# Performance work log

Measured on AMD Instinct MI355X. Metric: run time of the kernel, lower is better.

## Reference

```python
import jax, jax.numpy as jnp
import numpy as np

N, E, G = 10000, 160000, 64     # nodes, edges, graphs in batch
T, F_IN, F_OUT, L = 5, 75, 15, 4  # towers, per-tower in (divide_input=False), per-tower out, conv layers
AVG_DEG_LOG = float(np.log(17.0))  # stand-in for PyG histogram stat (source deg=zeros -> NaN)
BN_EPS = 1e-5
STD_EPS = 1e-5


def _u(key, shape):
    fi, fo = shape[-2], shape[-1]
    lim = float(np.sqrt(6.0 / (fi + fo)))
    return jax.random.uniform(key, shape, jnp.float32, -lim, lim)


def setup_inputs():
    key = jax.random.key(0)
    k = iter(jax.random.split(key, 24))
    inp = {}
    inp["x"] = jax.random.randint(next(k), (N, 2), 0, 21)
    inp["edge_index"] = jax.random.randint(next(k), (2, E), 0, N)
    inp["edge_attr"] = jax.random.randint(next(k), (E, 2), 0, 4)
    inp["batch"] = jnp.sort(jax.random.randint(next(k), (N,), 0, G))
    inp["node_emb"] = jax.random.normal(next(k), (21, 75), jnp.float32)
    inp["edge_emb"] = jax.random.normal(next(k), (4, 25), jnp.float32)
    inp["pre_lin_W"] = _u(next(k), (150, 75)); inp["pre_lin_b"] = jnp.zeros((75,), jnp.float32)
    inp["edge_enc_W"] = _u(next(k), (L, 50, F_IN)); inp["edge_enc_b"] = jnp.zeros((L, F_IN), jnp.float32)
    inp["pre_W"] = _u(next(k), (L, T, 3 * F_IN, F_IN)); inp["pre_b"] = jnp.zeros((L, T, F_IN), jnp.float32)
    inp["post_W"] = _u(next(k), (L, T, 13 * F_IN, F_OUT)); inp["post_b"] = jnp.zeros((L, T, F_OUT), jnp.float32)
    inp["lin_W"] = _u(next(k), (L, T * F_OUT, 75)); inp["lin_b"] = jnp.zeros((L, 75), jnp.float32)
    inp["bn_g"] = jnp.ones((L, 75), jnp.float32); inp["bn_b"] = jnp.zeros((L, 75), jnp.float32)
    inp["mlp_W1"] = _u(next(k), (75, 50)); inp["mlp_b1"] = jnp.zeros((50,), jnp.float32)
    inp["mlp_W2"] = _u(next(k), (50, 25)); inp["mlp_b2"] = jnp.zeros((25,), jnp.float32)
    inp["mlp_W3"] = _u(next(k), (25, 1)); inp["mlp_b3"] = jnp.zeros((1,), jnp.float32)
    return inp


def _forward(x, edge_index, edge_attr, batch, node_emb, edge_emb, pre_lin_W, pre_lin_b,
             edge_enc_W, edge_enc_b, pre_W, pre_b, post_W, post_b, lin_W, lin_b,
             bn_g, bn_b, mlp_W1, mlp_b1, mlp_W2, mlp_b2, mlp_W3, mlp_b3):
    # node / edge embeddings -> features
    h = node_emb[x].reshape(N, 150) @ pre_lin_W + pre_lin_b          # [N,75]
    ea = edge_emb[edge_attr].reshape(E, 50)                           # [E,50]
    src, dst = edge_index[0], edge_index[1]  # messages flow src -> dst (x_j=src, x_i=dst)

    cnt = jax.ops.segment_sum(jnp.ones((E,), jnp.float32), dst, num_segments=N)  # in-degree [N]
    deg = jnp.maximum(cnt, 1.0)[:, None, None]
    log_deg = jnp.log(jnp.maximum(cnt, 1.0) + 1.0)[:, None, None]
    amp = log_deg / AVG_DEG_LOG
    att = AVG_DEG_LOG / log_deg
    has = (cnt > 0)[:, None, None]

    for l in range(L):
        e = ea @ edge_enc_W[l] + edge_enc_b[l]                        # [E,75]
        m_in = jnp.concatenate([h[dst], h[src], e], axis=-1)          # [E,225]
        msgs = jnp.einsum('ec,tcf->etf', m_in, pre_W[l]) + pre_b[l]   # [E,T,75]
        s = jax.ops.segment_sum(msgs, dst, num_segments=N)
        mean = s / deg
        mean_sq = jax.ops.segment_sum(msgs * msgs, dst, num_segments=N) / deg
        std = jnp.sqrt(jax.nn.relu(mean_sq - mean * mean) + STD_EPS)
        mn = jnp.where(has, jax.ops.segment_min(msgs, dst, num_segments=N), 0.0)
        mx = jnp.where(has, jax.ops.segment_max(msgs, dst, num_segments=N), 0.0)
        agg = jnp.concatenate([mean, mn, mx, std], axis=-1)           # [N,T,300]
        scaled = jnp.concatenate([agg, agg * amp, agg * att], axis=-1)  # [N,T,900]
        out = jnp.concatenate([jnp.broadcast_to(h[:, None, :], (N, T, F_IN)), scaled], axis=-1)  # [N,T,975]
        post = jnp.einsum('ntc,tcf->ntf', out, post_W[l]) + post_b[l]  # [N,T,15]
        hc = post.reshape(N, T * F_OUT) @ lin_W[l] + lin_b[l]          # [N,75]
        mu = hc.mean(axis=0)
        var = hc.var(axis=0)  # biased, matches BatchNorm1d training mode
        h = jax.nn.relu((hc - mu) / jnp.sqrt(var + BN_EPS) * bn_g[l] + bn_b[l])

    g = jax.ops.segment_sum(h, batch, num_segments=G)                 # global_add_pool [G,75]
    g = jax.nn.relu(g @ mlp_W1 + mlp_b1)
    g = jax.nn.relu(g @ mlp_W2 + mlp_b2)
    return g @ mlp_W3 + mlp_b3                                        # [G,1]


def reference(x, edge_index, edge_attr, batch, node_emb, edge_emb, pre_lin_W, pre_lin_b,
              edge_enc_W, edge_enc_b, pre_W, pre_b, post_W, post_b, lin_W, lin_b,
              bn_g, bn_b, mlp_W1, mlp_b1, mlp_W2, mlp_b2, mlp_W3, mlp_b3):
    return _forward(x, edge_index, edge_attr, batch, node_emb, edge_emb, pre_lin_W, pre_lin_b,
                    edge_enc_W, edge_enc_b, pre_W, pre_b, post_W, post_b, lin_W, lin_b,
                    bn_g, bn_b, mlp_W1, mlp_b1, mlp_W2, mlp_b2, mlp_W3, mlp_b3)
```

## Files before the change

### kernel.cpp

```cpp
#include <hip/hip_runtime.h>
#include <hip/hip_bf16.h>
#include <math.h>

#define NN 10000
#define NE 160000
#define NG 64
#define NT 5
#define NL 4
#define ADL 2.833213344056216f

#define OFF_H      0
#define OFF_HC     750000
#define OFF_P      1500000
#define OFF_Q      5250000
#define OFF_AGG    9000000
#define OFF_RLUT   24000000
#define OFF_INVDEG 24006000
#define OFF_AMP    24016000
#define OFF_ATT    24026000
#define OFF_STATS  24036000
#define OFF_GPOOL  24036160
#define OFF_INT    24118960

__device__ __forceinline__ float bf2f(__hip_bfloat16 v){ return __bfloat162float(v); }

__global__ void k_zero_cnt(int* cnt){
    int i = blockIdx.x*256 + threadIdx.x;
    if (i < NN) cnt[i] = 0;
}

__global__ __launch_bounds__(256) void k_h0(const int* __restrict__ x,
        const float* __restrict__ node_emb, const float* __restrict__ plW,
        const float* __restrict__ plb, float* __restrict__ h){
    __shared__ float s_emb[21*75];
    __shared__ float s_W[150*75];
    __shared__ float s_b[75];
    int tid = threadIdx.x;
    for (int i = tid; i < 21*75; i += 256) s_emb[i] = node_emb[i];
    for (int i = tid; i < 150*75; i += 256) s_W[i] = plW[i];
    if (tid < 75) s_b[tid] = plb[tid];
    __syncthreads();
    for (int out = blockIdx.x*256 + tid; out < NN*75; out += gridDim.x*256){
        int n = out / 75, f = out - n*75;
        int x0 = x[2*n], x1 = x[2*n+1];
        float acc = s_b[f];
        const float* e0 = s_emb + x0*75;
        const float* e1 = s_emb + x1*75;
        #pragma unroll 5
        for (int k = 0; k < 75; k++)
            acc += e0[k]*s_W[k*75+f] + e1[k]*s_W[(75+k)*75+f];
        h[out] = acc;
    }
}

__global__ void k_hist(const int* __restrict__ ei, int* __restrict__ cnt){
    int e = blockIdx.x*256 + threadIdx.x;
    if (e < NE) atomicAdd(&cnt[ei[NE + e]], 1);
}

__global__ void k_scan(const int* __restrict__ cnt, int* __restrict__ eoff){
    __shared__ int buf[256];
    __shared__ int carry;
    int tid = threadIdx.x;
    if (tid == 0){ carry = 0; eoff[0] = 0; }
    __syncthreads();
    for (int base = 0; base < NN; base += 256){
        int v = (base + tid < NN) ? cnt[base + tid] : 0;
        buf[tid] = v; __syncthreads();
        for (int off = 1; off < 256; off <<= 1){
            int t2 = (tid >= off) ? buf[tid - off] : 0;
            __syncthreads();
            buf[tid] += t2;
            __syncthreads();
        }
        int inc = buf[tid] + carry;
        if (base + tid < NN) eoff[base + tid + 1] = inc;
        __syncthreads();
        if (tid == 255) carry = inc;
        __syncthreads();
    }
}

__global__ void k_nodestats(const int* __restrict__ cnt, const int* __restrict__ eoff,
        float* __restrict__ invdeg, float* __restrict__ amp, float* __restrict__ att,
        int* __restrict__ cursor){
    int n = blockIdx.x*256 + threadIdx.x;
    if (n >= NN) return;
    int c = cnt[n];
    cursor[n] = eoff[n];
    float cf = (float)c;
    float dg = cf < 1.f ? 1.f : cf;
    invdeg[n] = 1.f / dg;
    float ld = logf(dg + 1.f);
    amp[n] = ld / ADL;
    att[n] = ADL / ld;
}

__global__ void k_scatter(const int* __restrict__ ei, const int* __restrict__ ea,
        int* __restrict__ cursor, int* __restrict__ esrc, int* __restrict__ ecombo){
    int e = blockIdx.x*256 + threadIdx.x;
    if (e >= NE) return;
    int src = ei[e], dst = ei[NE + e];
    int pos = atomicAdd(&cursor[dst], 1);
    esrc[pos] = src;
    ecombo[pos] = ea[2*e]*4 + ea[2*e+1];
}

__global__ __launch_bounds__(384) void k_pq(const float* __restrict__ h,
        const float* __restrict__ preW, const float* __restrict__ preb,
        const float* __restrict__ edge_emb, const float* __restrict__ encW,
        const float* __restrict__ encb, int l,
        float* __restrict__ P, float* __restrict__ Q,
        float* __restrict__ Rlut, float* __restrict__ stats){
    __shared__ float smem[10675];
    int tid = threadIdx.x;
    int bx = blockIdx.x;

    if (bx == 318){
        for (int i = tid; i < 150; i += 384) stats[i] = 0.f;
        return;
    }
    if (bx >= 313){
        int t = bx - 313;
        float* s_encW = smem;
        float* s_ev   = smem + 3750;
        float* s_wc   = smem + 4950;
        float* s_ee   = smem + 10575;
        for (int i = tid; i < 3750; i += 384) s_encW[i] = encW[(size_t)l*3750 + i];
        for (int i = tid; i < 100; i += 384) s_ee[i] = edge_emb[i];
        const float* wcsrc = preW + (((size_t)(l*NT + t))*225 + 150)*75;
        for (int i = tid; i < 5625; i += 384) s_wc[i] = wcsrc[i];
        __syncthreads();
        for (int task = tid; task < 1200; task += 384){
            int b = task/75, m = task - 75*b;
            int a0 = b >> 2, a1 = b & 3;
            float s = encb[l*75 + m];
            for (int k = 0; k < 25; k++)
                s += s_ee[a0*25+k]*s_encW[k*75+m] + s_ee[a1*25+k]*s_encW[(25+k)*75+m];
            s_ev[task] = s;
        }
        __syncthreads();
        for (int task = tid; task < 1200; task += 384){
            int b = task/75, f = task - 75*b;
            float r = preb[((size_t)l*NT + t)*75 + f];
            const float* ev = s_ev + b*75;
            #pragma unroll 5
            for (int m = 0; m < 75; m++) r += ev[m]*s_wc[m*75 + f];
            Rlut[b*375 + t*75 + f] = r;
        }
        return;
    }

    float* h_t = smem;
    int base = bx*32;
    for (int idx = tid; idx < 32*75; idx += 384){
        int i = idx/75, m = idx - 75*i;
        int n = base + i;
        h_t[i*76 + m] = (n < NN) ? h[(size_t)n*75 + m] : 0.f;
    }
    __syncthreads();
    int j = tid;
    if (j >= 375) return;
    int t = j/75, f = j - 75*t;
    const float* wbase = preW + ((size_t)(l*NT + t))*225*75 + f;
    float accP[32], accQ[32];
    #pragma unroll
    for (int i = 0; i < 32; i++){ accP[i] = 0.f; accQ[i] = 0.f; }
    for (int m = 0; m < 72; m += 4){
        float wa0 = wbase[(m+0)*75], wa1 = wbase[(m+1)*75];
        float wa2 = wbase[(m+2)*75], wa3 = wbase[(m+3)*75];
        float wb0 = wbase[(75+m+0)*75], wb1 = wbase[(75+m+1)*75];
        float wb2 = wbase[(75+m+2)*75], wb3 = wbase[(75+m+3)*75];
        #pragma unroll
        for (int i = 0; i < 32; i++){
            const float4 hv = *(const float4*)&h_t[i*76 + m];
            accP[i] += hv.x*wa0 + hv.y*wa1 + hv.z*wa2 + hv.w*wa3;
            accQ[i] += hv.x*wb0 + hv.y*wb1 + hv.z*wb2 + hv.w*wb3;
        }
    }
    for (int m = 72; m < 75; m++){
        float wa = wbase[m*75], wb = wbase[(75+m)*75];
        #pragma unroll
        for (int i = 0; i < 32; i++){
            float v = h_t[i*76 + m];
            accP[i] += v*wa; accQ[i] += v*wb;
        }
    }
    for (int i = 0; i < 32; i++){
        int n = base + i;
        if (n < NN){ P[(size_t)n*375 + j] = accP[i]; Q[(size_t)n*375 + j] = accQ[i]; }
    }
}

#define JS 47
__global__ __launch_bounds__(64) void k_agg(const float* __restrict__ P,
        const float* __restrict__ Q, const float* __restrict__ Rlut,
        const int* __restrict__ eoff, const int* __restrict__ esrc,
        const int* __restrict__ ecombo, const float* __restrict__ invdeg,
        __hip_bfloat16* __restrict__ agg){
    int n = blockIdx.y;
    int j = blockIdx.x*JS + threadIdx.x;
    if (threadIdx.x >= JS || j >= 375) return;
    int lo = eoff[n], hi = eoff[n+1];
    float p = P[(size_t)n*375 + j];
    float sum = 0.f, sq = 0.f, mn = 3.4e38f, mx = -3.4e38f;
    int e = lo;
    for (; e + 4 <= hi; e += 4){
        int s0 = esrc[e],   s1 = esrc[e+1],   s2 = esrc[e+2],   s3 = esrc[e+3];
        int c0 = ecombo[e], c1 = ecombo[e+1], c2 = ecombo[e+2], c3 = ecombo[e+3];
        float q0 = Q[(size_t)s0*375 + j];
        float q1 = Q[(size_t)s1*375 + j];
        float q2 = Q[(size_t)s2*375 + j];
        float q3 = Q[(size_t)s3*375 + j];
        float r0 = Rlut[c0*375 + j];
        float r1 = Rlut[c1*375 + j];
        float r2 = Rlut[c2*375 + j];
        float r3 = Rlut[c3*375 + j];
        float m0 = p + q0 + r0, m1 = p + q1 + r1;
        float m2 = p + q2 + r2, m3 = p + q3 + r3;
        sum += m0 + m1 + m2 + m3;
        sq  += m0*m0 + m1*m1 + m2*m2 + m3*m3;
        mn = fminf(mn, fminf(fminf(m0, m1), fminf(m2, m3)));
        mx = fmaxf(mx, fmaxf(fmaxf(m0, m1), fmaxf(m2, m3)));
    }
    for (; e < hi; e++){
        int s = esrc[e], cm = ecombo[e];
        float m = p + Q[(size_t)s*375 + j] + Rlut[cm*375 + j];
        sum += m; sq += m*m;
        mn = fminf(mn, m); mx = fmaxf(mx, m);
    }
    float id = invdeg[n];
    bool has = hi > lo;
    float mean = sum*id;
    float msq  = sq*id;
    float var = msq - mean*mean; var = var > 0.f ? var : 0.f;
    float sd = sqrtf(var + 1e-5f);
    float mnv = has ? mn : 0.f;
    float mxv = has ? mx : 0.f;
    int t = j/75, f = j - 75*t;
    __hip_bfloat16* a = agg + ((size_t)n*NT + t)*300;
    a[f]      = __float2bfloat16(mean);
    a[75+f]   = __float2bfloat16(mnv);
    a[150+f]  = __float2bfloat16(mxv);
    a[225+f]  = __float2bfloat16(sd);
}

#define TK 25
#define PADA 27
__global__ __launch_bounds__(256, 4) void k_post(const float* __restrict__ h,
        const __hip_bfloat16* __restrict__ agg, const float* __restrict__ postW,
        const float* __restrict__ postb, const float* __restrict__ amp,
        const float* __restrict__ att, int l, float* __restrict__ postbase){
    __shared__ float s_a[256*PADA];
    __shared__ float s_w[3][TK*16];
    int t = blockIdx.y;
    int z = blockIdx.z;
    int nbase = blockIdx.x*256;
    int tid = threadIdx.x;
    int fg  = (tid & 3)*4;
    int sub = tid >> 2;
    const float* Wt = postW + ((size_t)(l*NT + t))*975*15;
    float a1[4][4], a2[4][4], a3[4][4];
    #pragma unroll
    for (int j = 0; j < 4; j++)
        #pragma unroll
        for (int f = 0; f < 4; f++){ a1[j][f]=0.f; a2[j][f]=0.f; a3[j][f]=0.f; }

    if (z == 0){
        for (int kt = 0; kt < 75; kt += TK){
            for (int idx = tid; idx < 256*TK; idx += 256){
                int row = idx / TK, c = idx - row*TK;
                int n = nbase + row;
                s_a[row*PADA + c] = (n < NN) ? h[(size_t)n*75 + kt + c] : 0.f;
            }
            for (int idx = tid; idx < TK*16; idx += 256){
                int c = idx >> 4, f = idx & 15;
                s_w[0][idx] = (f < 15) ? Wt[(kt + c)*15 + f] : 0.f;
            }
            __syncthreads();
            for (int k = 0; k < TK; k++){
                const float4 w1 = *(const float4*)&s_w[0][k*16 + fg];
                #pragma unroll
                for (int j = 0; j < 4; j++){
                    float v = s_a[(sub + 64*j)*PADA + k];
                    a1[j][0] += v*w1.x; a1[j][1] += v*w1.y;
                    a1[j][2] += v*w1.z; a1[j][3] += v*w1.w;
                }
            }
            __syncthreads();
        }
        const float* pb = postb + (l*NT + t)*15;
        #pragma unroll
        for (int j = 0; j < 4; j++){
            int n = nbase + sub + 64*j;
            if (n >= NN) continue;
            float* dst = postbase + (size_t)n*75 + t*15;
            #pragma unroll
            for (int f = 0; f < 4; f++)
                if (fg + f < 15) dst[fg + f] = a1[j][f] + pb[fg + f];
        }
        return;
    }

    int kbeg = (z-1)*50, kend = kbeg + 50;
    for (int kt = kbeg; kt < kend; kt += TK){
        for (int idx = tid; idx < 256*TK; idx += 256){
            int row = idx / TK, c = idx - row*TK;
            int n = nbase + row;
            s_a[row*PADA + c] = (n < NN) ?
                bf2f(agg[(size_t)n*1500 + t*300 + kt + c]) : 0.f;
        }
        for (int idx = tid; idx < TK*16; idx += 256){
            int c = idx >> 4, f = idx & 15;
            float v1 = 0.f, v2 = 0.f, v3 = 0.f;
            if (f < 15){
                v1 = Wt[( 75 + kt + c)*15 + f];
                v2 = Wt[(375 + kt + c)*15 + f];
                v3 = Wt[(675 + kt + c)*15 + f];
            }
            s_w[0][idx] = v1; s_w[1][idx] = v2; s_w[2][idx] = v3;
        }
        __syncthreads();
        for (int k = 0; k < TK; k++){
            const float4 w1 = *(const float4*)&s_w[0][k*16 + fg];
            const float4 w2 = *(const float4*)&s_w[1][k*16 + fg];
            const float4 w3 = *(const float4*)&s_w[2][k*16 + fg];
            #pragma unroll
            for (int j = 0; j < 4; j++){
                float v = s_a[(sub + 64*j)*PADA + k];
                a1[j][0] += v*w1.x; a1[j][1] += v*w1.y;
                a1[j][2] += v*w1.z; a1[j][3] += v*w1.w;
                a2[j][0] += v*w2.x; a2[j][1] += v*w2.y;
                a2[j][2] += v*w2.z; a2[j][3] += v*w2.w;
                a3[j][0] += v*w3.x; a3[j][1] += v*w3.y;
                a3[j][2] += v*w3.z; a3[j][3] += v*w3.w;
            }
        }
        __syncthreads();
    }

    float* postv = postbase + (size_t)z*750000;
    #pragma unroll
    for (int j = 0; j < 4; j++){
        int n = nbase + sub + 64*j;
        if (n >= NN) continue;
        float am = amp[n], at = att[n];
        float* dst = postv + (size_t)n*75 + t*15;
        #pragma unroll
        for (int f = 0; f < 4; f++)
            if (fg + f < 15)
                dst[fg + f] = a1[j][f] + am*a2[j][f] + at*a3[j][f];
    }
}

__global__ __launch_bounds__(256) void k_lin(const float* __restrict__ postbase,
        const float* __restrict__ linW, const float* __restrict__ linb,
        int l, float* __restrict__ hc, float* __restrict__ stats){
    __shared__ float p_l[32*75];
    __shared__ float w_l[75*75];
    __shared__ float hc_l[32*75];
    int tid = threadIdx.x;
    int base = blockIdx.x*32;
    for (int i = tid; i < 75*75; i += 256) w_l[i] = linW[(size_t)l*5625 + i];
    for (int i = tid; i < 32*75; i += 256){
        int n = base + i/75;
        size_t idx = (size_t)base*75 + i;
        float v = 0.f;
        if (n < NN){
            #pragma unroll
            for (int z = 0; z < 7; z++) v += postbase[idx + (size_t)z*750000];
        }
        p_l[i] = v;
    }
    __syncthreads();
    for (int task = tid; task < 2400; task += 256){
        int i = task/75, o = task - 75*i;
        float s = linb[l*75 + o];
        const float* pl = p_l + i*75;
        #pragma unroll 5
        for (int j = 0; j < 75; j++) s += pl[j]*w_l[j*75 + o];
        hc_l[task] = s;
        if (base + i < NN) hc[(size_t)(base+i)*75 + o] = s;
    }
    __syncthreads();
    if (tid < 75){
        int nv = NN - base; if (nv > 32) nv = 32;
        float s1 = 0.f, s2 = 0.f;
        for (int i = 0; i < nv; i++){
            float v = hc_l[i*75 + tid];
            s1 += v; s2 += v*v;
        }
        atomicAdd(&stats[tid], s1);
        atomicAdd(&stats[75+tid], s2);
    }
}

__global__ void k_bnapply(const float* __restrict__ hc, const float* __restrict__ stats,
        const float* __restrict__ bng, const float* __restrict__ bnb, int l,
        float* __restrict__ h){
    int idx = blockIdx.x*256 + threadIdx.x;
    if (idx >= NN*75) return;
    int col = idx % 75;
    float mu = stats[col]*(1.0f/NN);
    float var = stats[75+col]*(1.0f/NN) - mu*mu;
    float inv = rsqrtf(var + 1e-5f);
    float v = (hc[idx] - mu)*inv*bng[l*75+col] + bnb[l*75+col];
    h[idx] = v > 0.f ? v : 0.f;
}

__global__ __launch_bounds__(256) void k_pool(const float* __restrict__ h,
        const int* __restrict__ batch, float* __restrict__ gpool){
    int g = blockIdx.x, tid = threadIdx.x;
    int lo = 0, hi = NN;
    while (lo < hi){ int mid = (lo+hi)>>1; if (batch[mid] < g) lo = mid+1; else hi = mid; }
    int start = lo;
    lo = start; hi = NN;
    while (lo < hi){ int mid = (lo+hi)>>1; if (batch[mid] < g+1) lo = mid+1; else hi = mid; }
    int end = lo;
    __shared__ float red[225];
    if (tid < 225){
        int col = tid % 75, rep = tid / 75;
        float acc = 0.f;
        for (int i = start + rep; i < end; i += 3) acc += h[(size_t)i*75 + col];
        red[tid] = acc;
    }
    __syncthreads();
    if (tid < 75) gpool[g*75 + tid] = red[tid] + red[75+tid] + red[150+tid];
}

__global__ __launch_bounds__(256) void k_mlp(const float* __restrict__ gpool,
        const float* __restrict__ W1, const float* __restrict__ b1,
        const float* __restrict__ W2, const float* __restrict__ b2,
        const float* __restrict__ W3, const float* __restrict__ b3,
        float* __restrict__ out){
    __shared__ float w1[75*50];
    __shared__ float w2[50*25];
    __shared__ float gp[8*75];
    __shared__ float t1[8*50];
    __shared__ float t2[8*25];
    int tid = threadIdx.x;
    int gbase = blockIdx.x*8;
    for (int i = tid; i < 75*50; i += 256) w1[i] = W1[i];
    for (int i = tid; i < 50*25; i += 256) w2[i] = W2[i];
    for (int i = tid; i < 8*75; i += 256) gp[i] = gpool[gbase*75 + i];
    __syncthreads();
    for (int task = tid; task < 8*50; task += 256){
        int g = task/50, j = task - 50*g;
        float s = b1[j];
        const float* gv = gp + g*75;
        #pragma unroll 5
        for (int k = 0; k < 75; k++) s += gv[k]*w1[k*50+j];
        t1[task] = s > 0.f ? s : 0.f;
    }
    __syncthreads();
    for (int task = tid; task < 8*25; task += 256){
        int g = task/25, j = task - 25*g;
        float s = b2[j];
        const float* tv = t1 + g*50;
        #pragma unroll 5
        for (int k = 0; k < 50; k++) s += tv[k]*w2[k*25+j];
        t2[task] = s > 0.f ? s : 0.f;
    }
    __syncthreads();
    if (tid < 8){
        float s = b3[0];
        const float* tv = t2 + tid*25;
        #pragma unroll
        for (int k = 0; k < 25; k++) s += tv[k]*W3[k];
        out[gbase + tid] = s;
    }
}

extern "C" void kernel_launch(void* const* d_in, const int* in_sizes, int n_in,
                              void* d_out, int out_size, void* d_ws, size_t ws_size,
                              hipStream_t stream){
    const int* x          = (const int*)d_in[0];
    const int* edge_index = (const int*)d_in[1];
    const int* edge_attr  = (const int*)d_in[2];
    const int* batch      = (const int*)d_in[3];
    const float* node_emb = (const float*)d_in[4];
    const float* edge_emb = (const float*)d_in[5];
    const float* pre_lin_W= (const float*)d_in[6];
    const float* pre_lin_b= (const float*)d_in[7];
    const float* encW     = (const float*)d_in[8];
    const float* encb     = (const float*)d_in[9];
    const float* preW     = (const float*)d_in[10];
    const float* preb     = (const float*)d_in[11];
    const float* postW    = (const float*)d_in[12];
    const float* postb    = (const float*)d_in[13];
    const float* linW     = (const float*)d_in[14];
    const float* linb     = (const float*)d_in[15];
    const float* bng      = (const float*)d_in[16];
    const float* bnb      = (const float*)d_in[17];
    const float* mlpW1    = (const float*)d_in[18];
    const float* mlpb1    = (const float*)d_in[19];
    const float* mlpW2    = (const float*)d_in[20];
    const float* mlpb2    = (const float*)d_in[21];
    const float* mlpW3    = (const float*)d_in[22];
    const float* mlpb3    = (const float*)d_in[23];

    float* ws = (float*)d_ws;
    float* h      = ws + OFF_H;
    float* hc     = ws + OFF_HC;
    float* P      = ws + OFF_P;
    float* Q      = ws + OFF_Q;
    __hip_bfloat16* agg = (__hip_bfloat16*)(ws + OFF_AGG);
    float* Rlut   = ws + OFF_RLUT;
    float* invdeg = ws + OFF_INVDEG;
    float* amp    = ws + OFF_AMP;
    float* att    = ws + OFF_ATT;
    float* stats  = ws + OFF_STATS;
    float* gpool  = ws + OFF_GPOOL;
    float* postbase = ws + OFF_P;
    int* iw     = (int*)(ws + OFF_INT);
    int* cnt    = iw;
    int* eoff   = cnt + NN;
    int* cursor = eoff + NN + 2;
    int* esrc   = cursor + NN;
    int* ecombo = esrc + NE;

    k_zero_cnt<<<40, 256, 0, stream>>>(cnt);
    k_h0<<<640, 256, 0, stream>>>(x, node_emb, pre_lin_W, pre_lin_b, h);
    k_hist<<<625, 256, 0, stream>>>(edge_index, cnt);
    k_scan<<<1, 256, 0, stream>>>(cnt, eoff);
    k_nodestats<<<40, 256, 0, stream>>>(cnt, eoff, invdeg, amp, att, cursor);
    k_scatter<<<625, 256, 0, stream>>>(edge_index, edge_attr, cursor, esrc, ecombo);

    for (int l = 0; l < NL; l++){
        k_pq<<<319, 384, 0, stream>>>(h, preW, preb, edge_emb, encW, encb, l,
                                      P, Q, Rlut, stats);
        k_agg<<<dim3(8, NN), 64, 0, stream>>>(P, Q, Rlut, eoff, esrc, ecombo, invdeg, agg);
        k_post<<<dim3(40, 5, 7), 256, 0, stream>>>(h, agg, postW, postb, amp, att, l, postbase);
        k_lin<<<313, 256, 0, stream>>>(postbase, linW, linb, l, hc, stats);
        k_bnapply<<<2930, 256, 0, stream>>>(hc, stats, bng, bnb, l, h);
    }

    k_pool<<<NG, 256, 0, stream>>>(h, batch, gpool);
    k_mlp<<<8, 256, 0, stream>>>(gpool, mlpW1, mlpb1, mlpW2, mlpb2, mlpW3, mlpb3, (float*)d_out);
}
```

Baseline: 958.8 us.

## Store P/Q in bf16, widen agg unroll, drop LDS staging in post

The per-node pre-projections P and Q are now written and gathered as bf16 instead of fp32, halving the bytes moved by the gather-heavy aggregation kernel. The aggregation loop is unrolled to eight edges, and the grid uses full 64-thread blocks (6 per node) instead of 47 active lanes (8 per node). The post kernel stops staging activation tiles in shared memory and reads rows directly from global memory. Weights are loaded once into LDS and occupancy is raised to 6 blocks per CU. This trades extra rounding error in the messages, and uncoalesced per-thread row reads in the post kernel, for less memory traffic and fewer barriers.

```diff
diff --git a/kernel.cpp b/kernel.cpp
--- a/kernel.cpp
+++ b/kernel.cpp
@@ -110,7 +110,7 @@
         const float* __restrict__ preW, const float* __restrict__ preb,
         const float* __restrict__ edge_emb, const float* __restrict__ encW,
         const float* __restrict__ encb, int l,
-        float* __restrict__ P, float* __restrict__ Q,
+        __hip_bfloat16* __restrict__ P, __hip_bfloat16* __restrict__ Q,
         float* __restrict__ Rlut, float* __restrict__ stats){
     __shared__ float smem[10675];
     int tid = threadIdx.x;
@@ -188,44 +188,56 @@
     }
     for (int i = 0; i < 32; i++){
         int n = base + i;
-        if (n < NN){ P[(size_t)n*375 + j] = accP[i]; Q[(size_t)n*375 + j] = accQ[i]; }
-    }
-}
-
-#define JS 47
-__global__ __launch_bounds__(64) void k_agg(const float* __restrict__ P,
-        const float* __restrict__ Q, const float* __restrict__ Rlut,
+        if (n < NN){
+            P[(size_t)n*375 + j] = __float2bfloat16(accP[i]);
+            Q[(size_t)n*375 + j] = __float2bfloat16(accQ[i]);
+        }
+    }
+}
+
+__global__ __launch_bounds__(64) void k_agg(const __hip_bfloat16* __restrict__ P,
+        const __hip_bfloat16* __restrict__ Q, const float* __restrict__ Rlut,
         const int* __restrict__ eoff, const int* __restrict__ esrc,
         const int* __restrict__ ecombo, const float* __restrict__ invdeg,
         __hip_bfloat16* __restrict__ agg){
     int n = blockIdx.y;
-    int j = blockIdx.x*JS + threadIdx.x;
-    if (threadIdx.x >= JS || j >= 375) return;
+    int j = blockIdx.x*64 + threadIdx.x;
+    if (j >= 375) return;
     int lo = eoff[n], hi = eoff[n+1];
-    float p = P[(size_t)n*375 + j];
+    float p = bf2f(P[(size_t)n*375 + j]);
     float sum = 0.f, sq = 0.f, mn = 3.4e38f, mx = -3.4e38f;
     int e = lo;
-    for (; e + 4 <= hi; e += 4){
-        int s0 = esrc[e],   s1 = esrc[e+1],   s2 = esrc[e+2],   s3 = esrc[e+3];
-        int c0 = ecombo[e], c1 = ecombo[e+1], c2 = ecombo[e+2], c3 = ecombo[e+3];
-        float q0 = Q[(size_t)s0*375 + j];
-        float q1 = Q[(size_t)s1*375 + j];
-        float q2 = Q[(size_t)s2*375 + j];
-        float q3 = Q[(size_t)s3*375 + j];
-        float r0 = Rlut[c0*375 + j];
-        float r1 = Rlut[c1*375 + j];
-        float r2 = Rlut[c2*375 + j];
-        float r3 = Rlut[c3*375 + j];
+    for (; e + 8 <= hi; e += 8){
+        int s0 = esrc[e],   s1 = esrc[e+1], s2 = esrc[e+2], s3 = esrc[e+3];
+        int s4 = esrc[e+4], s5 = esrc[e+5], s6 = esrc[e+6], s7 = esrc[e+7];
+        int c0 = ecombo[e],   c1 = ecombo[e+1], c2 = ecombo[e+2], c3 = ecombo[e+3];
+        int c4 = ecombo[e+4], c5 = ecombo[e+5], c6 = ecombo[e+6], c7 = ecombo[e+7];
+        float q0 = bf2f(Q[(size_t)s0*375 + j]);
+        float q1 = bf2f(Q[(size_t)s1*375 + j]);
+        float q2 = bf2f(Q[(size_t)s2*375 + j]);
+        float q3 = bf2f(Q[(size_t)s3*375 + j]);
+        float q4 = bf2f(Q[(size_t)s4*375 + j]);
+        float q5 = bf2f(Q[(size_t)s5*375 + j]);
+        float q6 = bf2f(Q[(size_t)s6*375 + j]);
+        float q7 = bf2f(Q[(size_t)s7*375 + j]);
+        float r0 = Rlut[c0*375 + j], r1 = Rlut[c1*375 + j];
+        float r2 = Rlut[c2*375 + j], r3 = Rlut[c3*375 + j];
+        float r4 = Rlut[c4*375 + j], r5 = Rlut[c5*375 + j];
+        float r6 = Rlut[c6*375 + j], r7 = Rlut[c7*375 + j];
         float m0 = p + q0 + r0, m1 = p + q1 + r1;
         float m2 = p + q2 + r2, m3 = p + q3 + r3;
-        sum += m0 + m1 + m2 + m3;
-        sq  += m0*m0 + m1*m1 + m2*m2 + m3*m3;
-        mn = fminf(mn, fminf(fminf(m0, m1), fminf(m2, m3)));
-        mx = fmaxf(mx, fmaxf(fmaxf(m0, m1), fmaxf(m2, m3)));
+        float m4 = p + q4 + r4, m5 = p + q5 + r5;
+        float m6 = p + q6 + r6, m7 = p + q7 + r7;
+        sum += (m0 + m1 + m2 + m3) + (m4 + m5 + m6 + m7);
+        sq  += (m0*m0 + m1*m1 + m2*m2 + m3*m3) + (m4*m4 + m5*m5 + m6*m6 + m7*m7);
+        mn = fminf(mn, fminf(fminf(fminf(m0,m1), fminf(m2,m3)),
+                             fminf(fminf(m4,m5), fminf(m6,m7))));
+        mx = fmaxf(mx, fmaxf(fmaxf(fmaxf(m0,m1), fmaxf(m2,m3)),
+                             fmaxf(fmaxf(m4,m5), fmaxf(m6,m7))));
     }
     for (; e < hi; e++){
         int s = esrc[e], cm = ecombo[e];
-        float m = p + Q[(size_t)s*375 + j] + Rlut[cm*375 + j];
+        float m = p + bf2f(Q[(size_t)s*375 + j]) + Rlut[cm*375 + j];
         sum += m; sq += m*m;
         mn = fminf(mn, m); mx = fmaxf(mx, m);
     }
@@ -245,14 +257,12 @@
     a[225+f]  = __float2bfloat16(sd);
 }
 
-#define TK 25
-#define PADA 27
-__global__ __launch_bounds__(256, 4) void k_post(const float* __restrict__ h,
+#define KB2 50
+__global__ __launch_bounds__(256, 6) void k_post(const float* __restrict__ h,
         const __hip_bfloat16* __restrict__ agg, const float* __restrict__ postW,
         const float* __restrict__ postb, const float* __restrict__ amp,
         const float* __restrict__ att, int l, float* __restrict__ postbase){
-    __shared__ float s_a[256*PADA];
-    __shared__ float s_w[3][TK*16];
+    __shared__ float s_w[3*KB2*16];
     int t = blockIdx.y;
     int z = blockIdx.z;
     int nbase = blockIdx.x*256;
@@ -260,34 +270,29 @@
     int fg  = (tid & 3)*4;
     int sub = tid >> 2;
     const float* Wt = postW + ((size_t)(l*NT + t))*975*15;
-    float a1[4][4], a2[4][4], a3[4][4];
-    #pragma unroll
-    for (int j = 0; j < 4; j++)
-        #pragma unroll
-        for (int f = 0; f < 4; f++){ a1[j][f]=0.f; a2[j][f]=0.f; a3[j][f]=0.f; }
 
     if (z == 0){
-        for (int kt = 0; kt < 75; kt += TK){
-            for (int idx = tid; idx < 256*TK; idx += 256){
-                int row = idx / TK, c = idx - row*TK;
-                int n = nbase + row;
-                s_a[row*PADA + c] = (n < NN) ? h[(size_t)n*75 + kt + c] : 0.f;
+        for (int idx = tid; idx < 75*16; idx += 256){
+            int c = idx >> 4, f = idx & 15;
+            s_w[idx] = (f < 15) ? Wt[c*15 + f] : 0.f;
+        }
+        __syncthreads();
+        float a1[4][4] = {};
+        const float* hrow[4];
+        #pragma unroll
+        for (int j = 0; j < 4; j++){
+            int n = nbase + sub + 64*j;
+            hrow[j] = h + (size_t)(n < NN ? n : 0)*75;
+        }
+        #pragma unroll 3
+        for (int k = 0; k < 75; k++){
+            const float4 w1 = *(const float4*)&s_w[k*16 + fg];
+            #pragma unroll
+            for (int j = 0; j < 4; j++){
+                float v = hrow[j][k];
+                a1[j][0] += v*w1.x; a1[j][1] += v*w1.y;
+                a1[j][2] += v*w1.z; a1[j][3] += v*w1.w;
             }
-            for (int idx = tid; idx < TK*16; idx += 256){
-                int c = idx >> 4, f = idx & 15;
-                s_w[0][idx] = (f < 15) ? Wt[(kt + c)*15 + f] : 0.f;
-            }
-            __syncthreads();
-            for (int k = 0; k < TK; k++){
-                const float4 w1 = *(const float4*)&s_w[0][k*16 + fg];
-                #pragma unroll
-                for (int j = 0; j < 4; j++){
-                    float v = s_a[(sub + 64*j)*PADA + k];
-                    a1[j][0] += v*w1.x; a1[j][1] += v*w1.y;
-                    a1[j][2] += v*w1.z; a1[j][3] += v*w1.w;
-                }
-            }
-            __syncthreads();
         }
         const float* pb = postb + (l*NT + t)*15;
         #pragma unroll
@@ -302,43 +307,37 @@
         return;
     }
 
-    int kbeg = (z-1)*50, kend = kbeg + 50;
-    for (int kt = kbeg; kt < kend; kt += TK){
-        for (int idx = tid; idx < 256*TK; idx += 256){
-            int row = idx / TK, c = idx - row*TK;
-            int n = nbase + row;
-            s_a[row*PADA + c] = (n < NN) ?
-                bf2f(agg[(size_t)n*1500 + t*300 + kt + c]) : 0.f;
-        }
-        for (int idx = tid; idx < TK*16; idx += 256){
-            int c = idx >> 4, f = idx & 15;
-            float v1 = 0.f, v2 = 0.f, v3 = 0.f;
-            if (f < 15){
-                v1 = Wt[( 75 + kt + c)*15 + f];
-                v2 = Wt[(375 + kt + c)*15 + f];
-                v3 = Wt[(675 + kt + c)*15 + f];
-            }
-            s_w[0][idx] = v1; s_w[1][idx] = v2; s_w[2][idx] = v3;
-        }
-        __syncthreads();
-        for (int k = 0; k < TK; k++){
-            const float4 w1 = *(const float4*)&s_w[0][k*16 + fg];
-            const float4 w2 = *(const float4*)&s_w[1][k*16 + fg];
-            const float4 w3 = *(const float4*)&s_w[2][k*16 + fg];
-            #pragma unroll
-            for (int j = 0; j < 4; j++){
-                float v = s_a[(sub + 64*j)*PADA + k];
-                a1[j][0] += v*w1.x; a1[j][1] += v*w1.y;
-                a1[j][2] += v*w1.z; a1[j][3] += v*w1.w;
-                a2[j][0] += v*w2.x; a2[j][1] += v*w2.y;
-                a2[j][2] += v*w2.z; a2[j][3] += v*w2.w;
-                a3[j][0] += v*w3.x; a3[j][1] += v*w3.y;
-                a3[j][2] += v*w3.z; a3[j][3] += v*w3.w;
-            }
-        }
-        __syncthreads();
-    }
-
+    int kbeg = (z-1)*KB2;
+    for (int idx = tid; idx < 3*KB2*16; idx += 256){
+        int vrow = idx / (KB2*16);
+        int rem = idx - vrow*(KB2*16);
+        int c = rem >> 4, f = rem & 15;
+        s_w[idx] = (f < 15) ? Wt[(75 + vrow*300 + kbeg + c)*15 + f] : 0.f;
+    }
+    __syncthreads();
+    float a1[4][4] = {}, a2[4][4] = {}, a3[4][4] = {};
+    const __hip_bfloat16* arow[4];
+    #pragma unroll
+    for (int j = 0; j < 4; j++){
+        int n = nbase + sub + 64*j;
+        arow[j] = agg + (size_t)(n < NN ? n : 0)*1500 + t*300 + kbeg;
+    }
+    #pragma unroll 2
+    for (int k = 0; k < KB2; k++){
+        const float4 w1 = *(const float4*)&s_w[k*16 + fg];
+        const float4 w2 = *(const float4*)&s_w[(KB2 + k)*16 + fg];
+        const float4 w3 = *(const float4*)&s_w[(2*KB2 + k)*16 + fg];
+        #pragma unroll
+        for (int j = 0; j < 4; j++){
+            float v = bf2f(arow[j][k]);
+            a1[j][0] += v*w1.x; a1[j][1] += v*w1.y;
+            a1[j][2] += v*w1.z; a1[j][3] += v*w1.w;
+            a2[j][0] += v*w2.x; a2[j][1] += v*w2.y;
+            a2[j][2] += v*w2.z; a2[j][3] += v*w2.w;
+            a3[j][0] += v*w3.x; a3[j][1] += v*w3.y;
+            a3[j][2] += v*w3.z; a3[j][3] += v*w3.w;
+        }
+    }
     float* postv = postbase + (size_t)z*750000;
     #pragma unroll
     for (int j = 0; j < 4; j++){
@@ -502,8 +501,8 @@
     float* ws = (float*)d_ws;
     float* h      = ws + OFF_H;
     float* hc     = ws + OFF_HC;
-    float* P      = ws + OFF_P;
-    float* Q      = ws + OFF_Q;
+    __hip_bfloat16* P = (__hip_bfloat16*)(ws + OFF_P);
+    __hip_bfloat16* Q = (__hip_bfloat16*)(ws + OFF_Q);
     __hip_bfloat16* agg = (__hip_bfloat16*)(ws + OFF_AGG);
     float* Rlut   = ws + OFF_RLUT;
     float* invdeg = ws + OFF_INVDEG;
@@ -529,7 +528,7 @@
     for (int l = 0; l < NL; l++){
         k_pq<<<319, 384, 0, stream>>>(h, preW, preb, edge_emb, encW, encb, l,
                                       P, Q, Rlut, stats);
-        k_agg<<<dim3(8, NN), 64, 0, stream>>>(P, Q, Rlut, eoff, esrc, ecombo, invdeg, agg);
+        k_agg<<<dim3(6, NN), 64, 0, stream>>>(P, Q, Rlut, eoff, esrc, ecombo, invdeg, agg);
         k_post<<<dim3(40, 5, 7), 256, 0, stream>>>(h, agg, postW, postb, amp, att, l, postbase);
         k_lin<<<313, 256, 0, stream>>>(postbase, linW, linb, l, hc, stats);
         k_bnapply<<<2930, 256, 0, stream>>>(hc, stats, bng, bnb, l, h);
```

After: 919.4 us. -4.1%, faster.
